# Kernel optimization log

Hardware: AMD Instinct MI355X
Metric: run time of the kernel (lower is better)

## Reference

```python
import jax, jax.numpy as jnp
import numpy as np

C = 512
HEADS = 8
HEAD_DIM = C // HEADS
GROUPS = 32
EPS = 1e-5


def group_norm(x, scale, bias):
    b, c, h, w = x.shape
    xg = x.reshape(b, GROUPS, -1)
    mean = xg.mean(axis=-1, keepdims=True)
    var = xg.var(axis=-1, keepdims=True)
    xg = (xg - mean) * jax.lax.rsqrt(var + EPS)
    x = xg.reshape(b, c, h, w)
    return x * scale[None, :, None, None] + bias[None, :, None, None]


def conv1x1(x, w, b):
    # w: (out_c, in_c), x: (B, C, H, W)
    return jnp.einsum('oc,bchw->bohw', w, x) + b[None, :, None, None]


def setup_inputs() -> dict:
    key = jax.random.key(0)
    ks = jax.random.split(key, 11)
    s = 1.0 / np.sqrt(C)
    return {
        'x': jax.random.normal(ks[0], (8, C, 32, 32), jnp.float32),
        'gn_scale': jnp.ones((C,), jnp.float32),
        'gn_bias': jnp.zeros((C,), jnp.float32),
        'wq': jax.random.normal(ks[1], (C, C), jnp.float32) * s,
        'bq': jax.random.normal(ks[2], (C,), jnp.float32) * 0.01,
        'wk': jax.random.normal(ks[3], (C, C), jnp.float32) * s,
        'bk': jax.random.normal(ks[4], (C,), jnp.float32) * 0.01,
        'wv': jax.random.normal(ks[5], (C, C), jnp.float32) * s,
        'bv': jax.random.normal(ks[6], (C,), jnp.float32) * 0.01,
        'wp': jax.random.normal(ks[7], (C, C), jnp.float32) * s,
        'bp': jax.random.normal(ks[8], (C,), jnp.float32) * 0.01,
    }


def reference(x, gn_scale, gn_bias, wq, bq, wk, bk, wv, bv, wp, bp):
    b, c, h, w = x.shape
    n = h * w
    h_in = x
    xn = group_norm(x, gn_scale, gn_bias)
    q = conv1x1(xn, wq, bq).reshape(b, HEADS, HEAD_DIM, n)
    k = conv1x1(xn, wk, bk).reshape(b, HEADS, HEAD_DIM, n)
    v = conv1x1(xn, wv, bv).reshape(b, HEADS, HEAD_DIM, n)
    scale = 1.0 / np.sqrt(HEAD_DIM).astype(np.float32)
    attn = jnp.einsum('bhcn,bhcm->bhnm', q, k) * scale
    attn = jax.nn.softmax(attn, axis=-1)
    out = jnp.einsum('bhnm,bhcm->bhcn', attn, v)
    out = out.reshape(b, c, h, w)
    out = conv1x1(out, wp, bp)
    return out + h_in
```

## Files before the change

### kernel.cpp

```cpp
#include <hip/hip_runtime.h>

#define CC 512
#define NN 1024
#define NB 8
#define NH 8
#define HD 64

typedef __attribute__((ext_vector_type(8))) short s16x8;
typedef __attribute__((ext_vector_type(4))) short s16x4;
typedef __attribute__((ext_vector_type(4))) float f32x4;
typedef __attribute__((ext_vector_type(16))) float f32x16;

__device__ __forceinline__ unsigned cvtpk(float lo, float hi){
  unsigned r;
  asm("v_cvt_pk_bf16_f32 %0, %1, %2" : "=v"(r) : "v"(lo), "v"(hi));
  return r;
}

__device__ __forceinline__ s16x4 pack4(float a, float b, float c, float d){
  union { unsigned u[2]; s16x4 v; } r;
  r.u[0] = cvtpk(a, b);
  r.u[1] = cvtpk(c, d);
  return r.v;
}

__device__ __forceinline__ void gload16(const void* g, void* l){
  __builtin_amdgcn_global_load_lds((const __attribute__((address_space(1))) void*)g,
                                   (__attribute__((address_space(3))) void*)l, 16, 0, 0);
}

__global__ __launch_bounds__(256) void prep_kernel(const float* __restrict__ x,
    const float* __restrict__ gsc, const float* __restrict__ gbi,
    const float* __restrict__ w0, const float* __restrict__ w1,
    const float* __restrict__ w2, const float* __restrict__ w3,
    short* __restrict__ wbf, short* __restrict__ xnt){
  if (blockIdx.x < 1024){
    const int i = blockIdx.x*256 + threadIdx.x;
    const int sel = i >> 16;
    const int off = (i & 65535) << 2;
    const float* src = (sel==0) ? w0 : (sel==1) ? w1 : (sel==2) ? w2 : w3;
    const float4 v = *reinterpret_cast<const float4*>(src + off);
    *reinterpret_cast<s16x4*>(wbf + (size_t)sel*262144 + off) = pack4(v.x, v.y, v.z, v.w);
    return;
  }
  const int blk = blockIdx.x - 1024;
  const int b = blk >> 5;
  const int g = blk & 31;
  const int t = threadIdx.x;
  const float* base = x + ((size_t)b*CC + g*16)*NN;
  float4 vals[16];
  float s = 0.f, s2 = 0.f;
  #pragma unroll
  for (int k = 0; k < 16; ++k){
    float4 v = *reinterpret_cast<const float4*>(base + k*NN + t*4);
    vals[k] = v;
    s  += v.x + v.y + v.z + v.w;
    s2 += v.x*v.x + v.y*v.y + v.z*v.z + v.w*v.w;
  }
  #pragma unroll
  for (int m = 1; m < 64; m <<= 1){ s += __shfl_xor(s, m); s2 += __shfl_xor(s2, m); }
  __shared__ float rs[4], rs2[4];
  const int wid = t >> 6, lane = t & 63;
  if (lane == 0){ rs[wid] = s; rs2[wid] = s2; }
  __syncthreads();
  s  = rs[0] + rs[1] + rs[2] + rs[3];
  s2 = rs2[0] + rs2[1] + rs2[2] + rs2[3];
  const float mean = s * (1.f/16384.f);
  const float inv = rsqrtf(s2 * (1.f/16384.f) - mean*mean + 1e-5f);
  float scl[16], off[16];
  #pragma unroll
  for (int k = 0; k < 16; ++k){
    const float sc = gsc[g*16 + k] * inv;
    scl[k] = sc;
    off[k] = gbi[g*16 + k] - mean * sc;
  }
  short* obase = xnt + ((size_t)b*NN + t*4)*CC + g*16;
  #pragma unroll
  for (int i = 0; i < 4; ++i){
    float fv[16];
    #pragma unroll
    for (int k = 0; k < 16; ++k){
      const float v = (i==0) ? vals[k].x : (i==1) ? vals[k].y : (i==2) ? vals[k].z : vals[k].w;
      fv[k] = v * scl[k] + off[k];
    }
    union { unsigned u[4]; s16x8 v; } lo, hi;
    #pragma unroll
    for (int j = 0; j < 4; ++j){
      lo.u[j] = cvtpk(fv[2*j],     fv[2*j + 1]);
      hi.u[j] = cvtpk(fv[8 + 2*j], fv[8 + 2*j + 1]);
    }
    *reinterpret_cast<s16x8*>(obase + (size_t)i*CC)     = lo.v;
    *reinterpret_cast<s16x8*>(obase + (size_t)i*CC + 8) = hi.v;
  }
}

template<int MODE>
__global__ __launch_bounds__(256) void gemm_kernel(
    const short* __restrict__ Wb, const short* __restrict__ Bmat,
    const float* __restrict__ bias0, const float* __restrict__ bias1, const float* __restrict__ bias2,
    const float* __restrict__ resid,
    short* __restrict__ qt, short* __restrict__ kt2, short* __restrict__ vo,
    float* __restrict__ outp)
{
  const int w = blockIdx.x;
  const int nt = w & 7;
  const int s = w >> 3;
  const int batch = s & 7;
  int mt, z;
  if (MODE == 0){ const int r = s >> 3; mt = r & 3; z = r >> 2; }
  else          { mt = s >> 3; z = 0; }
  const int tid = threadIdx.x;
  const int lane = tid & 63, wid = tid >> 6;
  const int wm = wid >> 1, wn = wid & 1;

  __shared__ short As[128*64];
  __shared__ short Bs[128*64];

  const short* Wz = Wb + (size_t)(MODE == 0 ? z : 3) * 262144;
  const short* Brow = Bmat + ((size_t)batch*NN + nt*128)*CC;

  const f32x4 fzero = {0.f, 0.f, 0.f, 0.f};
  f32x4 acc[4][4];
  #pragma unroll
  for (int i = 0; i < 4; ++i)
  #pragma unroll
  for (int j = 0; j < 4; ++j)
    acc[i][j] = fzero;

  for (int kk = 0; kk < 8; ++kk){
    __syncthreads();
    #pragma unroll
    for (int j = 0; j < 4; ++j){
      const int id = tid + 256*j;
      const int row = id >> 3, ch = id & 7;
      const int gch = ch ^ (row & 7);
      gload16(Wz   + (size_t)(mt*128 + row)*CC + kk*64 + gch*8, As + (wid*64 + 256*j)*8);
      gload16(Brow + (size_t)row*CC          + kk*64 + gch*8, Bs + (wid*64 + 256*j)*8);
    }
    __syncthreads();
    #pragma unroll
    for (int ks = 0; ks < 2; ++ks){
      s16x8 a[4], b[4];
      #pragma unroll
      for (int mi = 0; mi < 4; ++mi){
        const int row = wm*64 + mi*16 + (lane & 15);
        const int ch = (ks*4 + (lane >> 4)) ^ (row & 7);
        a[mi] = *reinterpret_cast<const s16x8*>(&As[row*64 + ch*8]);
      }
      #pragma unroll
      for (int ni = 0; ni < 4; ++ni){
        const int row = wn*64 + ni*16 + (lane & 15);
        const int ch = (ks*4 + (lane >> 4)) ^ (row & 7);
        b[ni] = *reinterpret_cast<const s16x8*>(&Bs[row*64 + ch*8]);
      }
      if (MODE == 0 && z == 2){
        #pragma unroll
        for (int mi = 0; mi < 4; ++mi)
        #pragma unroll
        for (int ni = 0; ni < 4; ++ni)
          acc[mi][ni] = __builtin_amdgcn_mfma_f32_16x16x32_bf16(b[ni], a[mi], acc[mi][ni], 0, 0, 0);
      } else {
        #pragma unroll
        for (int mi = 0; mi < 4; ++mi)
        #pragma unroll
        for (int ni = 0; ni < 4; ++ni)
          acc[mi][ni] = __builtin_amdgcn_mfma_f32_16x16x32_bf16(a[mi], b[ni], acc[mi][ni], 0, 0, 0);
      }
    }
  }

  const int obase = mt*128 + wm*64;
  const int nbase = nt*128 + wn*64;
  if (MODE == 0){
    const int head = mt*2 + wm;
    const size_t hb = ((size_t)batch*NH + head)*65536;
    const int hi2 = (lane >> 5) & 1;
    const int j0 = ((lane >> 4) & 1)*4;
    if (z < 2){
      const float* bias = (z == 0) ? bias0 : bias1;
      short* dst = (z == 0) ? qt : kt2;
      const float qs = (z == 0) ? 0.125f * 1.44269504f : 1.0f;
      #pragma unroll
      for (int mi = 0; mi < 4; ++mi){
        float bv4[4];
        #pragma unroll
        for (int r = 0; r < 4; ++r) bv4[r] = bias[obase + mi*16 + (lane>>4)*4 + r];
        #pragma unroll
        for (int ni = 0; ni < 4; ++ni){
          const int l = (ni & 1)*16 + (lane & 15) + 32*hi2;
          const int q5 = nt*4 + wn*2 + (ni >> 1);
          const s16x4 pk = pack4((acc[mi][ni][0] + bv4[0]) * qs,
                                 (acc[mi][ni][1] + bv4[1]) * qs,
                                 (acc[mi][ni][2] + bv4[2]) * qs,
                                 (acc[mi][ni][3] + bv4[3]) * qs);
          *reinterpret_cast<s16x4*>(dst + hb + (size_t)((q5*4 + mi)*64 + l)*8 + j0) = pk;
        }
      }
    } else {
      #pragma unroll
      for (int mi = 0; mi < 4; ++mi){
        const float bv = bias2[obase + mi*16 + (lane & 15)];
        const int ci = mi >> 1;
        const int cl = (mi & 1)*16 + (lane & 15);
        #pragma unroll
        for (int ni = 0; ni < 4; ++ni){
          const int m5 = nt*2 + wn;
          const s16x4 pk = pack4(acc[mi][ni][0] + bv, acc[mi][ni][1] + bv,
                                 acc[mi][ni][2] + bv, acc[mi][ni][3] + bv);
          *reinterpret_cast<s16x4*>(vo + hb + (size_t)((((ci*16 + m5)*4 + ni)*64) + cl + 32*hi2)*8 + j0) = pk;
        }
      }
    }
  } else {
    #pragma unroll
    for (int mi = 0; mi < 4; ++mi){
      float bv4[4];
      #pragma unroll
      for (int r = 0; r < 4; ++r) bv4[r] = bias0[obase + mi*16 + (lane>>4)*4 + r];
      #pragma unroll
      for (int ni = 0; ni < 4; ++ni){
        const int n = nbase + ni*16 + (lane & 15);
        #pragma unroll
        for (int r = 0; r < 4; ++r){
          const int o = obase + mi*16 + (lane>>4)*4 + r;
          const size_t idx = ((size_t)batch*CC + o)*NN + n;
          outp[idx] = acc[mi][ni][r] + bv4[r] + resid[idx];
        }
      }
    }
  }
}

__global__ __launch_bounds__(256, 2) void attn_kernel(
    const short* __restrict__ qp, const short* __restrict__ kp, const short* __restrict__ vp,
    short* __restrict__ ot)
{
  const int bid = blockIdx.x;
  const int xcd = bid & 7, rr = bid >> 3;
  const int bh  = xcd*8 + (rr & 7);
  const int qt  = rr >> 3;
  const int b = bh >> 3, head = bh & 7;
  const int tid = threadIdx.x, lane = tid & 63, wid = tid >> 6;
  const int col = lane & 31;
  const int qg = wid & 1, kh = wid >> 1;
  const int q0 = qt*64 + qg*32;

  const short* Qf = qp + (size_t)bh*65536;
  const short* Kf = kp + (size_t)bh*65536;
  const short* Vf = vp + (size_t)bh*65536;

  __shared__ float Lof[2][32][64];
  __shared__ float Ll[2][64];

  const int q5 = qt*2 + qg;
  s16x8 qf[4];
  #pragma unroll
  for (int ks = 0; ks < 4; ++ks)
    qf[ks] = *reinterpret_cast<const s16x8*>(Qf + (size_t)(q5*4 + ks)*512 + lane*8);

  f32x16 of0, of1;
  #pragma unroll
  for (int r = 0; r < 16; ++r){ of0[r] = 0.f; of1[r] = 0.f; }
  float l = 0.f;

  auto kload = [&](int itn, s16x8 (&kf)[2][4]){
    const short* kb = Kf + (size_t)(kh*16 + itn*2)*2048 + lane*8;
    #pragma unroll
    for (int t = 0; t < 2; ++t)
      #pragma unroll
      for (int ks = 0; ks < 4; ++ks)
        kf[t][ks] = *reinterpret_cast<const s16x8*>(kb + t*2048 + ks*512);
  };

  auto pack = [&](f32x16& sv, s16x8& p0, s16x8& p1){
    union { unsigned u[4]; s16x8 v; } w0, w1;
    {
      unsigned a = cvtpk(sv[0], sv[1]);
      unsigned c = cvtpk(sv[4], sv[5]);
      auto r = __builtin_amdgcn_permlane32_swap(a, c, false, false);
      w0.u[0] = r[0]; w0.u[2] = r[1];
      a = cvtpk(sv[2], sv[3]);
      c = cvtpk(sv[6], sv[7]);
      r = __builtin_amdgcn_permlane32_swap(a, c, false, false);
      w0.u[1] = r[0]; w0.u[3] = r[1];
    }
    {
      unsigned a = cvtpk(sv[8], sv[9]);
      unsigned c = cvtpk(sv[12], sv[13]);
      auto r = __builtin_amdgcn_permlane32_swap(a, c, false, false);
      w1.u[0] = r[0]; w1.u[2] = r[1];
      a = cvtpk(sv[10], sv[11]);
      c = cvtpk(sv[14], sv[15]);
      r = __builtin_amdgcn_permlane32_swap(a, c, false, false);
      w1.u[1] = r[0]; w1.u[3] = r[1];
    }
    p0 = w0.v; p1 = w1.v;
  };

  auto body = [&](int it, s16x8 (&kf)[2][4], s16x8 (&kfn)[2][4]){
    const int m5 = kh*8 + it;
    s16x8 vf[2][4];
    const short* vb = Vf + (size_t)m5*2048 + lane*8;
    #pragma unroll
    for (int ci = 0; ci < 2; ++ci)
      #pragma unroll
      for (int s = 0; s < 4; ++s)
        vf[ci][s] = *reinterpret_cast<const s16x8*>(vb + ci*32768 + s*512);
    f32x16 s0, s1;
    #pragma unroll
    for (int r = 0; r < 16; ++r){ s0[r] = 0.f; s1[r] = 0.f; }
    #pragma unroll
    for (int ks = 0; ks < 4; ++ks){
      s0 = __builtin_amdgcn_mfma_f32_32x32x16_bf16(kf[0][ks], qf[ks], s0, 0, 0, 0);
      s1 = __builtin_amdgcn_mfma_f32_32x32x16_bf16(kf[1][ks], qf[ks], s1, 0, 0, 0);
    }
    if (it < 7) kload(it + 1, kfn);
    #pragma unroll
    for (int r = 0; r < 16; ++r){ s0[r] = __builtin_amdgcn_exp2f(s0[r]); }
    #pragma unroll
    for (int r = 0; r < 16; ++r){ s1[r] = __builtin_amdgcn_exp2f(s1[r]); }
    float t[16];
    #pragma unroll
    for (int r = 0; r < 16; ++r) t[r] = s0[r] + s1[r];
    #pragma unroll
    for (int o = 8; o > 0; o >>= 1)
      #pragma unroll
      for (int r = 0; r < 8; ++r) if (r < o) t[r] = t[r] + t[r + o];
    l += t[0] + __shfl_xor(t[0], 32);
    s16x8 pf[4];
    pack(s0, pf[0], pf[1]);
    pack(s1, pf[2], pf[3]);
    #pragma unroll
    for (int s = 0; s < 4; ++s){
      of0 = __builtin_amdgcn_mfma_f32_32x32x16_bf16(vf[0][s], pf[s], of0, 0, 0, 0);
      of1 = __builtin_amdgcn_mfma_f32_32x32x16_bf16(vf[1][s], pf[s], of1, 0, 0, 0);
    }
  };

  s16x8 kfA[2][4], kfB[2][4];
  kload(0, kfA);
  #pragma unroll 1
  for (int ii = 0; ii < 4; ++ii){
    body(2*ii,     kfA, kfB);
    body(2*ii + 1, kfB, kfA);
  }

  __syncthreads();
  if (kh == 1){
    #pragma unroll
    for (int r = 0; r < 16; ++r){
      Lof[qg][r][lane]      = of0[r];
      Lof[qg][16 + r][lane] = of1[r];
    }
    Ll[qg][lane] = l;
  }
  __syncthreads();
  if (kh == 0){
    const float linv = 1.f / (l + Ll[qg][lane]);
    const int hi = lane >> 5;
    const int n = q0 + col;
    short* ob = ot + ((size_t)b*NN + n)*CC + head*HD + hi*4;
    #pragma unroll
    for (int rq = 0; rq < 4; ++rq){
      s16x4 pk = pack4((of0[rq*4 + 0] + Lof[qg][rq*4 + 0][lane]) * linv,
                       (of0[rq*4 + 1] + Lof[qg][rq*4 + 1][lane]) * linv,
                       (of0[rq*4 + 2] + Lof[qg][rq*4 + 2][lane]) * linv,
                       (of0[rq*4 + 3] + Lof[qg][rq*4 + 3][lane]) * linv);
      *reinterpret_cast<s16x4*>(ob + rq*8) = pk;
      pk = pack4((of1[rq*4 + 0] + Lof[qg][16 + rq*4 + 0][lane]) * linv,
                 (of1[rq*4 + 1] + Lof[qg][16 + rq*4 + 1][lane]) * linv,
                 (of1[rq*4 + 2] + Lof[qg][16 + rq*4 + 2][lane]) * linv,
                 (of1[rq*4 + 3] + Lof[qg][16 + rq*4 + 3][lane]) * linv);
      *reinterpret_cast<s16x4*>(ob + 32 + rq*8) = pk;
    }
  }
}

extern "C" void kernel_launch(void* const* d_in, const int* in_sizes, int n_in,
                              void* d_out, int out_size, void* d_ws, size_t ws_size,
                              hipStream_t stream) {
  const float* x   = (const float*)d_in[0];
  const float* gsc = (const float*)d_in[1];
  const float* gbi = (const float*)d_in[2];
  const float* wq  = (const float*)d_in[3];
  const float* bq  = (const float*)d_in[4];
  const float* wk  = (const float*)d_in[5];
  const float* bk  = (const float*)d_in[6];
  const float* wv  = (const float*)d_in[7];
  const float* bv  = (const float*)d_in[8];
  const float* wp  = (const float*)d_in[9];
  const float* bp  = (const float*)d_in[10];
  float* out = (float*)d_out;

  char* ws = (char*)d_ws;
  short* wbf = (short*)(ws);
  short* xnt = (short*)(ws + (2u<<20));
  short* qt  = (short*)(ws + (10u<<20));
  short* kt  = (short*)(ws + (18u<<20));
  short* v   = (short*)(ws + (26u<<20));
  short* aot = (short*)(ws + (34u<<20));

  prep_kernel<<<1280, 256, 0, stream>>>(x, gsc, gbi, wq, wk, wv, wp, wbf, xnt);
  gemm_kernel<0><<<dim3(768), 256, 0, stream>>>(wbf, xnt, bq, bk, bv, nullptr,
                                                qt, kt, v, nullptr);
  attn_kernel<<<dim3(1024), 256, 0, stream>>>(qt, kt, v, aot);
  gemm_kernel<1><<<dim3(256), 256, 0, stream>>>(wbf, aot, bp, nullptr, nullptr, x,
                                                nullptr, nullptr, nullptr, out);
}
```

Before: 76.66 us.

## Double-buffer GEMM K-loop with BK=32 and vectorize output-projection epilogue

Rewrites the GEMM main loop to use two 128x32 LDS buffers per operand, prefetching the next K slice while MFMAs run on the current one, with one barrier per step instead of two. The XOR swizzle is adapted to the 32-wide tile. For the output projection it also swaps the MFMA operand order so each lane holds four consecutive n values, which allows float4 loads of the residual and float4 stores of the output instead of scalar accesses. This adds more loop iterations and a waitcnt/barrier per step, and keeps the same LDS footprint.

Measured after the change: 76.74 us. No clear change (+0.1%).

```diff
diff --git a/kernel.cpp b/kernel.cpp
--- a/kernel.cpp
+++ b/kernel.cpp
@@ -113,8 +113,8 @@
   const int lane = tid & 63, wid = tid >> 6;
   const int wm = wid >> 1, wn = wid & 1;
 
-  __shared__ short As[128*64];
-  __shared__ short Bs[128*64];
+  __shared__ short As[2][128*32];
+  __shared__ short Bs[2][128*32];
 
   const short* Wz = Wb + (size_t)(MODE == 0 ? z : 3) * 262144;
   const short* Brow = Bmat + ((size_t)batch*NN + nt*128)*CC;
@@ -127,46 +127,62 @@
   for (int j = 0; j < 4; ++j)
     acc[i][j] = fzero;
 
-  for (int kk = 0; kk < 8; ++kk){
-    __syncthreads();
-    #pragma unroll
-    for (int j = 0; j < 4; ++j){
-      const int id = tid + 256*j;
-      const int row = id >> 3, ch = id & 7;
-      const int gch = ch ^ (row & 7);
-      gload16(Wz   + (size_t)(mt*128 + row)*CC + kk*64 + gch*8, As + (wid*64 + 256*j)*8);
-      gload16(Brow + (size_t)row*CC          + kk*64 + gch*8, Bs + (wid*64 + 256*j)*8);
-    }
-    __syncthreads();
-    #pragma unroll
-    for (int ks = 0; ks < 2; ++ks){
-      s16x8 a[4], b[4];
-      #pragma unroll
-      for (int mi = 0; mi < 4; ++mi){
-        const int row = wm*64 + mi*16 + (lane & 15);
-        const int ch = (ks*4 + (lane >> 4)) ^ (row & 7);
-        a[mi] = *reinterpret_cast<const s16x8*>(&As[row*64 + ch*8]);
-      }
-      #pragma unroll
-      for (int ni = 0; ni < 4; ++ni){
-        const int row = wn*64 + ni*16 + (lane & 15);
-        const int ch = (ks*4 + (lane >> 4)) ^ (row & 7);
-        b[ni] = *reinterpret_cast<const s16x8*>(&Bs[row*64 + ch*8]);
-      }
-      if (MODE == 0 && z == 2){
-        #pragma unroll
-        for (int mi = 0; mi < 4; ++mi)
-        #pragma unroll
-        for (int ni = 0; ni < 4; ++ni)
-          acc[mi][ni] = __builtin_amdgcn_mfma_f32_16x16x32_bf16(b[ni], a[mi], acc[mi][ni], 0, 0, 0);
-      } else {
-        #pragma unroll
-        for (int mi = 0; mi < 4; ++mi)
-        #pragma unroll
-        for (int ni = 0; ni < 4; ++ni)
-          acc[mi][ni] = __builtin_amdgcn_mfma_f32_16x16x32_bf16(a[mi], b[ni], acc[mi][ni], 0, 0, 0);
-      }
-    }
+  const int srow = tid >> 2, sh = tid & 3;
+  const int sg = sh ^ ((srow >> 1) & 3);
+  const short* gaBase = Wz + (size_t)(mt*128 + srow)*CC + sg*8;
+  const short* gbBase = Brow + (size_t)srow*CC + sg*8;
+
+  auto stage = [&](int kk, int buf){
+    const short* ga = gaBase + kk*32;
+    const short* gb = gbBase + kk*32;
+    gload16(ga,         &As[buf][tid*8]);
+    gload16(ga + 64*CC, &As[buf][(tid + 256)*8]);
+    gload16(gb,         &Bs[buf][tid*8]);
+    gload16(gb + 64*CC, &Bs[buf][(tid + 256)*8]);
+  };
+
+  const int rch = (lane >> 4) ^ (((lane & 15) >> 1) & 3);
+
+  auto compute = [&](int buf){
+    s16x8 a[4], b[4];
+    #pragma unroll
+    for (int mi = 0; mi < 4; ++mi){
+      const int row = wm*64 + mi*16 + (lane & 15);
+      a[mi] = *reinterpret_cast<const s16x8*>(&As[buf][row*32 + rch*8]);
+    }
+    #pragma unroll
+    for (int ni = 0; ni < 4; ++ni){
+      const int row = wn*64 + ni*16 + (lane & 15);
+      b[ni] = *reinterpret_cast<const s16x8*>(&Bs[buf][row*32 + rch*8]);
+    }
+    if (MODE == 1 || (MODE == 0 && z == 2)){
+      #pragma unroll
+      for (int mi = 0; mi < 4; ++mi)
+      #pragma unroll
+      for (int ni = 0; ni < 4; ++ni)
+        acc[mi][ni] = __builtin_amdgcn_mfma_f32_16x16x32_bf16(b[ni], a[mi], acc[mi][ni], 0, 0, 0);
+    } else {
+      #pragma unroll
+      for (int mi = 0; mi < 4; ++mi)
+      #pragma unroll
+      for (int ni = 0; ni < 4; ++ni)
+        acc[mi][ni] = __builtin_amdgcn_mfma_f32_16x16x32_bf16(a[mi], b[ni], acc[mi][ni], 0, 0, 0);
+    }
+  };
+
+  stage(0, 0);
+  asm volatile("s_waitcnt vmcnt(0)" ::: "memory");
+  __builtin_amdgcn_s_barrier();
+  int buf = 0;
+  #pragma unroll
+  for (int kk = 0; kk < 16; ++kk){
+    if (kk < 15) stage(kk + 1, buf ^ 1);
+    compute(buf);
+    if (kk < 15){
+      asm volatile("s_waitcnt vmcnt(0)" ::: "memory");
+      __builtin_amdgcn_s_barrier();
+    }
+    buf ^= 1;
   }
 
   const int obase = mt*128 + wm*64;
@@ -214,18 +230,19 @@
   } else {
     #pragma unroll
     for (int mi = 0; mi < 4; ++mi){
-      float bv4[4];
-      #pragma unroll
-      for (int r = 0; r < 4; ++r) bv4[r] = bias0[obase + mi*16 + (lane>>4)*4 + r];
+      const int o = obase + mi*16 + (lane & 15);
+      const float bv = bias0[o];
       #pragma unroll
       for (int ni = 0; ni < 4; ++ni){
-        const int n = nbase + ni*16 + (lane & 15);
-        #pragma unroll
-        for (int r = 0; r < 4; ++r){
-          const int o = obase + mi*16 + (lane>>4)*4 + r;
-          const size_t idx = ((size_t)batch*CC + o)*NN + n;
-          outp[idx] = acc[mi][ni][r] + bv4[r] + resid[idx];
-        }
+        const int n4 = nbase + ni*16 + (lane >> 4)*4;
+        const size_t idx = ((size_t)batch*CC + o)*NN + n4;
+        const float4 rv = *reinterpret_cast<const float4*>(resid + idx);
+        float4 ov;
+        ov.x = acc[mi][ni][0] + bv + rv.x;
+        ov.y = acc[mi][ni][1] + bv + rv.y;
+        ov.z = acc[mi][ni][2] + bv + rv.z;
+        ov.w = acc[mi][ni][3] + bv + rv.w;
+        *reinterpret_cast<float4*>(outp + idx) = ov;
       }
     }
   }
```
